# Performance work log

Measured on AMD Instinct MI355X. Metric: run time of the kernel, lower is better.

## Reference

```python
import jax, jax.numpy as jnp
import numpy as np

NUM_HEADS = 8
EMBED_CH = 512   # k channels
OUT_CH = 256     # v channels
MASK_CURRENT = False
NEG_INF = -1e30


def setup_inputs() -> dict:
    key = jax.random.key(0)
    ks = jax.random.split(key, 7)
    N, C, H, W = 8, 256, 32, 32
    s = lambda fan: 1.0 / np.sqrt(fan)
    return {
        "x": jax.random.normal(ks[0], (N, C, H, W), jnp.float32),
        "Wq": jax.random.normal(ks[1], (EMBED_CH, C), jnp.float32) * s(C),
        "bq": jax.random.normal(ks[2], (EMBED_CH,), jnp.float32) * 0.01,
        "Wkv": jax.random.normal(ks[3], (EMBED_CH + OUT_CH, C), jnp.float32) * s(C),
        "bkv": jax.random.normal(ks[4], (EMBED_CH + OUT_CH,), jnp.float32) * 0.01,
        "Wo": jax.random.normal(ks[5], (OUT_CH, OUT_CH), jnp.float32) * s(OUT_CH),
        "bo": jax.random.normal(ks[6], (OUT_CH,), jnp.float32) * 0.01,
    }


def _to_multihead(t, n, T):
    # t: [n, h*d, T] with channel layout '(h d)' -> [n, h, T, d]
    h = NUM_HEADS
    return t.reshape(n, h, -1, T).transpose(0, 1, 3, 2)


def reference(x, Wq, bq, Wkv, bkv, Wo, bo):
    n, C, H, W = x.shape
    T = H * W
    xf = x.reshape(n, C, T)  # flatten spatial dims into sequence

    # 1x1 convs == pointwise channel GEMMs
    q = jnp.einsum('oc,nct->not', Wq, xf) + bq[None, :, None]
    kv = jnp.einsum('oc,nct->not', Wkv, xf) + bkv[None, :, None]
    k, v = kv[:, :EMBED_CH], kv[:, EMBED_CH:]

    q = _to_multihead(q, n, T)   # [n, h, T, dk]
    k = _to_multihead(k, n, T)   # [n, h, T, dk]
    v = _to_multihead(v, n, T)   # [n, h, T, dv]

    dk = k.shape[-1]
    scale = 1.0 / np.sqrt(dk).astype(np.float32)

    # causal mask over flattened spatial positions (lower-triangular)
    diag = -1 if MASK_CURRENT else 0
    mask = jnp.tril(jnp.ones((T, T), dtype=bool), k=diag)  # [T, T]

    attn = jnp.einsum('nhtd,nhsd->nhts', q, k) * scale
    attn = jnp.where(mask[None, None], attn, NEG_INF)
    attn = jax.nn.softmax(attn, axis=-1)
    attn = jnp.where(mask[None, None], attn, 0.0)

    out = jnp.einsum('nhts,nhsd->nhtd', attn, v)            # [n, h, T, dv]
    out = out.transpose(0, 1, 3, 2).reshape(n, OUT_CH, T)   # n (h d) t

    out = jnp.einsum('oc,nct->not', Wo, out) + bo[None, :, None]
    return out.reshape(n, OUT_CH, H, W)
```

## Files before the change

### kernel.cpp

```cpp
#include <hip/hip_runtime.h>
#include <hip/hip_bf16.h>
#include <math.h>

typedef __bf16 bf16;
typedef __attribute__((ext_vector_type(4))) __bf16 bf16x4;
typedef __attribute__((ext_vector_type(8))) __bf16 bf16x8;
typedef __attribute__((ext_vector_type(4))) float f32x4;

#define T_DIM 1024
#define C_DIM 256
#define HEADS 8

static __device__ __forceinline__ int tb(int row, int col) {
  return row * 128 + ((((col >> 3) ^ row) & 7) << 4) + ((col & 7) << 1);
}

__global__ __launch_bounds__(256) void k_prep(const float* __restrict__ x,
    const float* __restrict__ Wq, const float* __restrict__ Wkv, const float* __restrict__ Wo,
    char* __restrict__ xTt, char* __restrict__ Wbt, char* __restrict__ Wot) {
  const int tid = threadIdx.x;
  const int b = blockIdx.x;
  if (b < 512) {
    __shared__ float tile[64][65];
    const int n = b >> 6, rem = b & 63, tt64 = rem >> 2, ct = (rem & 3) << 6;
    const float* xp = x + ((size_t)n * C_DIM + ct) * T_DIM + tt64 * 64;
    const int t4 = (tid & 15) * 4, c0 = tid >> 4;
#pragma unroll
    for (int i = 0; i < 4; ++i) {
      const int c = c0 + i * 16;
      float4 v = *(const float4*)(xp + (size_t)c * T_DIM + t4);
      tile[c][t4] = v.x; tile[c][t4 + 1] = v.y; tile[c][t4 + 2] = v.z; tile[c][t4 + 3] = v.w;
    }
    __syncthreads();
    char* dst = xTt + (((size_t)(n * 8 + (tt64 >> 1))) * 4 + (rem & 3)) * 16384;
    const int rbase = (tt64 & 1) * 64;
#pragma unroll
    for (int i = 0; i < 2; ++i) {
      const int idx = tid + i * 256;
      const int tl = idx >> 3, c8 = (idx & 7) * 8;
      bf16x8 v;
#pragma unroll
      for (int j = 0; j < 8; ++j) v[j] = (bf16)tile[c8 + j][tl];
      *(bf16x8*)(dst + tb(rbase + tl, c8)) = v;
    }
  } else {
    const bool isWo = (b >= 532);
    const int o0 = (b - (isWo ? 532 : 512)) * 64;
#pragma unroll
    for (int i = 0; i < 8; ++i) {
      const int idx = tid + i * 256;
      const int row = idx >> 5, c8 = (idx & 31) * 8;
      const int o = o0 + row;
      const float* src = isWo ? (Wo + (size_t)o * C_DIM + c8)
                              : (o < 512 ? Wq + (size_t)o * C_DIM + c8
                                         : Wkv + (size_t)(o - 512) * C_DIM + c8);
      float4 a = *(const float4*)src;
      float4 bq4 = *(const float4*)(src + 4);
      bf16x8 v;
      v[0]=(bf16)a.x; v[1]=(bf16)a.y; v[2]=(bf16)a.z; v[3]=(bf16)a.w;
      v[4]=(bf16)bq4.x; v[5]=(bf16)bq4.y; v[6]=(bf16)bq4.z; v[7]=(bf16)bq4.w;
      char* base = isWo ? Wot : Wbt;
      char* dst = base + (((size_t)(o >> 7)) * 4 + (c8 >> 6)) * 16384;
      *(bf16x8*)(dst + tb(o & 127, c8 & 63)) = v;
    }
  }
}

__global__ __launch_bounds__(256) void k_qkv(const char* __restrict__ Wbt, const char* __restrict__ xTt,
    const float* __restrict__ bq, const float* __restrict__ bkv,
    bf16* __restrict__ q_ws, char* __restrict__ Kt, char* __restrict__ Vt) {
  __shared__ __attribute__((aligned(128))) unsigned char smem[34816];
  const int tid = threadIdx.x;
  const int nt = blockIdx.x, mt = blockIdx.y, n = blockIdx.z;
  const int w = tid >> 6, lane = tid & 63, lrow = lane & 15, lg = lane >> 4;
  const int wm = (w >> 1) * 64, wn = (w & 1) * 64;
  const char* gA = Wbt + (size_t)mt * 65536;
  const char* gB = xTt + ((size_t)(n * 8 + nt)) * 65536;
  const float s2 = 0.18033688f;
  const int coff = w * 1024 + lane * 16;

  bf16x8 sA0, sA1, sA2, sA3, sB0, sB1, sB2, sB3;
  auto issue = [&](int kk) {
    const char* a = gA + kk * 16384 + coff;
    sA0 = *(const bf16x8*)(a);         sA1 = *(const bf16x8*)(a + 4096);
    sA2 = *(const bf16x8*)(a + 8192);  sA3 = *(const bf16x8*)(a + 12288);
    const char* bsrc = gB + kk * 16384 + coff;
    sB0 = *(const bf16x8*)(bsrc);        sB1 = *(const bf16x8*)(bsrc + 4096);
    sB2 = *(const bf16x8*)(bsrc + 8192); sB3 = *(const bf16x8*)(bsrc + 12288);
  };

  f32x4 acc[4][4] = {};
  issue(0);
#pragma unroll 1
  for (int kk = 0; kk < 4; ++kk) {
    __syncthreads();
    char* da = (char*)smem + coff;
    *(bf16x8*)(da)         = sA0; *(bf16x8*)(da + 4096)  = sA1;
    *(bf16x8*)(da + 8192)  = sA2; *(bf16x8*)(da + 12288) = sA3;
    char* db = (char*)smem + 16384 + coff;
    *(bf16x8*)(db)         = sB0; *(bf16x8*)(db + 4096)  = sB1;
    *(bf16x8*)(db + 8192)  = sB2; *(bf16x8*)(db + 12288) = sB3;
    if (kk < 3) issue(kk + 1);
    __syncthreads();
    const char* As = (const char*)smem;
    const char* Bs = As + 16384;
    bf16x8 af[4][2], bv[4][2];
#pragma unroll
    for (int mi = 0; mi < 4; ++mi)
#pragma unroll
      for (int kh = 0; kh < 2; ++kh)
        af[mi][kh] = *(const bf16x8*)(As + tb(wm + mi * 16 + lrow, kh * 32 + lg * 8));
#pragma unroll
    for (int ni = 0; ni < 4; ++ni)
#pragma unroll
      for (int kh = 0; kh < 2; ++kh)
        bv[ni][kh] = *(const bf16x8*)(Bs + tb(wn + ni * 16 + lrow, kh * 32 + lg * 8));
#pragma unroll
    for (int kh = 0; kh < 2; ++kh)
#pragma unroll
      for (int mi = 0; mi < 4; ++mi)
#pragma unroll
        for (int ni = 0; ni < 4; ++ni)
          acc[mi][ni] = __builtin_amdgcn_mfma_f32_16x16x32_bf16(af[mi][kh], bv[ni][kh], acc[mi][ni], 0, 0, 0);
  }
  __syncthreads();

  const int obase = mt * 128 + wm + lg * 4;
  const int tcol0 = nt * 128 + wn + lrow;
  if (mt < 8) {
#pragma unroll
    for (int mi = 0; mi < 4; ++mi) {
      const int o = obase + mi * 16;
      if (mt < 4) {
        const float4 bb = *(const float4*)(bq + o);
        const int nh = n * 8 + (o >> 6), d = o & 63;
        bf16* qrow = q_ws + (size_t)nh * (T_DIM * 64) + d;
#pragma unroll
        for (int ni = 0; ni < 4; ++ni) {
          const int t = tcol0 + ni * 16;
          f32x4 v = acc[mi][ni];
          bf16x4 pk;
          pk[0]=(bf16)((v[0]+bb.x)*s2); pk[1]=(bf16)((v[1]+bb.y)*s2);
          pk[2]=(bf16)((v[2]+bb.z)*s2); pk[3]=(bf16)((v[3]+bb.w)*s2);
          *(bf16x4*)(qrow + (size_t)t * 64) = pk;
        }
      } else {
        const int o2 = o - 512;
        const float4 bb = *(const float4*)(bkv + o2);
        const int nh = n * 8 + (o2 >> 6), d = o2 & 63;
        char* tbase = Kt + (size_t)nh * 16 * 8192;
#pragma unroll
        for (int ni = 0; ni < 4; ++ni) {
          const int t = tcol0 + ni * 16;
          f32x4 v = acc[mi][ni];
          bf16x4 pk;
          pk[0]=(bf16)(v[0]+bb.x); pk[1]=(bf16)(v[1]+bb.y); pk[2]=(bf16)(v[2]+bb.z); pk[3]=(bf16)(v[3]+bb.w);
          *(bf16x4*)(tbase + (t >> 6) * 8192 + tb(t & 63, d)) = pk;
        }
      }
    }
  } else {
    bf16* tp = (bf16*)smem;
#pragma unroll
    for (int mi = 0; mi < 4; ++mi) {
      const int o3g = (mt - 8) * 128 + wm + mi * 16 + lg * 4;
      const float4 bb = *(const float4*)(bkv + 512 + o3g);
      const float* bbp = (const float*)&bb;
      const int o3l = wm + mi * 16 + lg * 4;
#pragma unroll
      for (int ni = 0; ni < 4; ++ni) {
        const int tl = wn + ni * 16 + lrow;
        f32x4 v = acc[mi][ni];
#pragma unroll
        for (int r = 0; r < 4; ++r)
          tp[(o3l + r) * 132 + tl] = (bf16)(v[r] + bbp[r]);
      }
    }
    __syncthreads();
    const int row = tid >> 1, half = tid & 1;
    const int o3 = (mt - 8) * 128 + row;
    const int nh = n * 8 + (o3 >> 5), dv = o3 & 31;
    char* tile = Vt + (size_t)nh * 16 * 4096 + (nt * 2 + half) * 4096;
    const bf16* src = tp + row * 132 + half * 64;
#pragma unroll
    for (int g = 0; g < 8; ++g) {
      bf16x4 lo = *(const bf16x4*)(src + g * 8);
      bf16x4 hi = *(const bf16x4*)(src + g * 8 + 4);
      bf16x8 vv;
      vv[0]=lo[0]; vv[1]=lo[1]; vv[2]=lo[2]; vv[3]=lo[3];
      vv[4]=hi[0]; vv[5]=hi[1]; vv[6]=hi[2]; vv[7]=hi[3];
      *(bf16x8*)(tile + tb(dv, g * 8)) = vv;
    }
  }
}

__global__ __launch_bounds__(256) void k_attn(const bf16* __restrict__ q_ws,
    const char* __restrict__ Kt, const char* __restrict__ Vt, char* __restrict__ attTt) {
  __shared__ __attribute__((aligned(128))) unsigned char smem[32768];
  const int tid = threadIdx.x;
  const int nh = blockIdx.x, qt = blockIdx.y;
  const int w = tid >> 6, lane = tid & 63, lrow = lane & 15, lg = lane >> 4;
  const int tl = w * 16 + lrow;
  const char* Ktb = Kt + (size_t)nh * 16 * 8192;
  const char* Vtb = Vt + (size_t)nh * 16 * 4096;
  const int n = nh >> 3, h = nh & 7;
  const int coff = tid * 16;

  const int tg = qt * 64 + tl;
  const bf16* qb = q_ws + ((size_t)nh * T_DIM + tg) * 64;
  const bf16x8 qf0 = *(const bf16x8*)(qb + lg * 8);
  const bf16x8 qf1 = *(const bf16x8*)(qb + 32 + lg * 8);

  float l = 0.f;
  f32x4 oa = {}, ob = {};

  bf16x8 s0, s1, s2, s3, s4, s5;
  auto issue = [&](int st2, bool has1) {
    const char* k0 = Ktb + (size_t)st2 * 8192 + coff;
    s0 = *(const bf16x8*)(k0);
    s1 = *(const bf16x8*)(k0 + 4096);
    s4 = *(const bf16x8*)(Vtb + (size_t)st2 * 4096 + coff);
    if (has1) {
      s2 = *(const bf16x8*)(k0 + 8192);
      s3 = *(const bf16x8*)(k0 + 12288);
      s5 = *(const bf16x8*)(Vtb + (size_t)(st2 + 1) * 4096 + coff);
    }
  };

  issue(0, 1 <= qt);
#pragma unroll 1
  for (int st2 = 0; st2 <= qt; st2 += 2) {
    const bool has1 = (st2 + 1 <= qt);
    __syncthreads();
    {
      char* kd = (char*)smem + coff;
      *(bf16x8*)(kd) = s0;
      *(bf16x8*)(kd + 4096) = s1;
      *(bf16x8*)((char*)smem + 16384 + coff) = s4;
      if (has1) {
        *(bf16x8*)(kd + 8192) = s2;
        *(bf16x8*)(kd + 12288) = s3;
        *(bf16x8*)((char*)smem + 20480 + coff) = s5;
      }
    }
    const int nst2 = st2 + 2;
    if (nst2 <= qt) issue(nst2, nst2 + 1 <= qt);
    __syncthreads();
    const int nsub = has1 ? 2 : 1;
#pragma unroll 1
    for (int sub = 0; sub < nsub; ++sub) {
      const int stk = st2 + sub;
      const char* Kbs = (const char*)smem + sub * 8192;
      const char* Vbs = (const char*)smem + 16384 + sub * 4096;
      char* pws = (char*)smem + 24576 + w * 2048;
      const bool diag = (stk == qt);

      f32x4 sacc[4];
      __builtin_amdgcn_s_setprio(1);
#pragma unroll
      for (int rt = 0; rt < 4; ++rt) {
        f32x4 a = {0.f, 0.f, 0.f, 0.f};
        bf16x8 kf0 = *(const bf16x8*)(Kbs + tb(rt * 16 + lrow, lg * 8));
        a = __builtin_amdgcn_mfma_f32_16x16x32_bf16(kf0, qf0, a, 0, 0, 0);
        bf16x8 kf1 = *(const bf16x8*)(Kbs + tb(rt * 16 + lrow, 32 + lg * 8));
        a = __builtin_amdgcn_mfma_f32_16x16x32_bf16(kf1, qf1, a, 0, 0, 0);
        sacc[rt] = a;
      }
      __builtin_amdgcn_s_setprio(0);
      float p[16];
#pragma unroll
      for (int rt = 0; rt < 4; ++rt)
#pragma unroll
        for (int r = 0; r < 4; ++r) {
          float e = __builtin_amdgcn_exp2f(sacc[rt][r]);
          if (diag && (rt * 16 + lg * 4 + r) > tl) e = 0.f;
          p[rt * 4 + r] = e;
        }
      float t0 = (p[0] + p[1]) + (p[2] + p[3]);
      float t1 = (p[4] + p[5]) + (p[6] + p[7]);
      float t2 = (p[8] + p[9]) + (p[10] + p[11]);
      float t3 = (p[12] + p[13]) + (p[14] + p[15]);
      float ps = (t0 + t1) + (t2 + t3);
      ps += __shfl_xor(ps, 16);
      ps += __shfl_xor(ps, 32);
      l += ps;
#pragma unroll
      for (int rt = 0; rt < 4; ++rt) {
        bf16x4 pk;
#pragma unroll
        for (int r = 0; r < 4; ++r) pk[r] = (bf16)p[rt * 4 + r];
        *(bf16x4*)(pws + tb(lrow, rt * 16 + lg * 4)) = pk;
      }
      __builtin_amdgcn_s_setprio(1);
#pragma unroll
      for (int ks = 0; ks < 2; ++ks) {
        bf16x8 pf = *(const bf16x8*)(pws + tb(lrow, ks * 32 + lg * 8));
        bf16x8 vf0 = *(const bf16x8*)(Vbs + tb(lrow, ks * 32 + lg * 8));
        oa = __builtin_amdgcn_mfma_f32_16x16x32_bf16(vf0, pf, oa, 0, 0, 0);
        bf16x8 vf1 = *(const bf16x8*)(Vbs + tb(16 + lrow, ks * 32 + lg * 8));
        ob = __builtin_amdgcn_mfma_f32_16x16x32_bf16(vf1, pf, ob, 0, 0, 0);
      }
      __builtin_amdgcn_s_setprio(0);
    }
  }

  const float inv = 1.0f / l;
  const int ntt = tg >> 7, row = tg & 127;
#pragma unroll
  for (int dt = 0; dt < 2; ++dt) {
    const f32x4 v = dt ? ob : oa;
    const int c = h * 32 + dt * 16 + lg * 4;
    char* tile = attTt + (((size_t)(n * 8 + ntt)) * 4 + (c >> 6)) * 16384;
    bf16x4 pk;
#pragma unroll
    for (int r = 0; r < 4; ++r) pk[r] = (bf16)(v[r] * inv);
    *(bf16x4*)(tile + tb(row, c & 63)) = pk;
  }
}

__global__ __launch_bounds__(256) void k_proj(const char* __restrict__ attTt,
    const char* __restrict__ Wot, const float* __restrict__ bo, float* __restrict__ out) {
  __shared__ __attribute__((aligned(128))) unsigned char smem[12288];
  const int tid = threadIdx.x;
  const int tm = blockIdx.x, om = blockIdx.y, n = blockIdx.z;
  const int w = tid >> 6, lane = tid & 63, lrow = lane & 15, lg = lane >> 4;
  const int wm = (w >> 1) * 16, wn = (w & 1) * 32;
  const char* gA = attTt + ((size_t)(n * 8 + (tm >> 2))) * 65536 + (tm & 3) * 4096;
  const char* gB = Wot + (size_t)(om >> 1) * 65536 + (om & 1) * 8192;
  const int coff = tid * 16;

  bf16x8 pA0, pB0, pB1;
  auto issue = [&](int kk) {
    pA0 = *(const bf16x8*)(gA + kk * 16384 + coff);
    const char* bsrc = gB + kk * 16384 + coff;
    pB0 = *(const bf16x8*)(bsrc); pB1 = *(const bf16x8*)(bsrc + 4096);
  };

  f32x4 acc[2] = {};
  issue(0);
#pragma unroll 1
  for (int kk = 0; kk < 4; ++kk) {
    __syncthreads();
    if (coff < 4096) *(bf16x8*)((char*)smem + coff) = pA0;
    char* db = (char*)smem + 4096 + coff;
    *(bf16x8*)(db) = pB0; *(bf16x8*)(db + 4096) = pB1;
    if (kk < 3) issue(kk + 1);
    __syncthreads();
    const char* As = (const char*)smem;
    const char* Bs = As + 4096;
    bf16x8 af[2], bv[2][2];
#pragma unroll
    for (int kh = 0; kh < 2; ++kh)
      af[kh] = *(const bf16x8*)(As + tb(wm + lrow, kh * 32 + lg * 8));
#pragma unroll
    for (int ni = 0; ni < 2; ++ni)
#pragma unroll
      for (int kh = 0; kh < 2; ++kh)
        bv[ni][kh] = *(const bf16x8*)(Bs + tb(wn + ni * 16 + lrow, kh * 32 + lg * 8));
#pragma unroll
    for (int kh = 0; kh < 2; ++kh)
#pragma unroll
      for (int ni = 0; ni < 2; ++ni)
        acc[ni] = __builtin_amdgcn_mfma_f32_16x16x32_bf16(af[kh], bv[ni][kh], acc[ni], 0, 0, 0);
  }

  const int t0 = tm * 32 + wm + lg * 4;
#pragma unroll
  for (int ni = 0; ni < 2; ++ni) {
    const int o = om * 64 + wn + ni * 16 + lrow;
    const float bb = bo[o];
    f32x4 v = acc[ni];
    v[0] += bb; v[1] += bb; v[2] += bb; v[3] += bb;
    *(f32x4*)(out + ((size_t)(n * C_DIM + o)) * T_DIM + t0) = v;
  }
}

extern "C" void kernel_launch(void* const* d_in, const int* in_sizes, int n_in,
                              void* d_out, int out_size, void* d_ws, size_t ws_size,
                              hipStream_t stream) {
  const float* x   = (const float*)d_in[0];
  const float* Wq  = (const float*)d_in[1];
  const float* bq  = (const float*)d_in[2];
  const float* Wkv = (const float*)d_in[3];
  const float* bkv = (const float*)d_in[4];
  const float* Wo  = (const float*)d_in[5];
  const float* bo  = (const float*)d_in[6];
  float* out = (float*)d_out;

  char* ws = (char*)d_ws;
  char* xTt   = ws;
  char* Wbt   = ws + (4u  << 20);
  char* Wot   = ws + (5u  << 20);
  bf16* q_ws  = (bf16*)(ws + (6u << 20));
  char* Kt    = ws + (14u << 20);
  char* Vt    = ws + (22u << 20);
  char* attTt = ws + (26u << 20);

  k_prep<<<536, 256, 0, stream>>>(x, Wq, Wkv, Wo, xTt, Wbt, Wot);
  k_qkv<<<dim3(8, 10, 8), 256, 0, stream>>>(Wbt, xTt, bq, bkv, q_ws, Kt, Vt);
  k_attn<<<dim3(64, 16), 256, 0, stream>>>(q_ws, Kt, Vt, attTt);
  k_proj<<<dim3(32, 4, 8), 256, 0, stream>>>(attTt, Wot, bo, out);
}
```

Before: 52.44 us.

## Pair causal query tiles per block and read K/V and proj operands directly from global

The attention kernel now gives each block two query tiles (qp and 15-qp), so every block does about the same amount of causal work, and the grid is halved. Each K/V tile is loaded once and used for both query tiles. The LDS staging and its __syncthreads barriers are removed: K/V fragments are read straight from global memory, and LDS holds only the P tiles. The output projection kernel likewise drops LDS staging and reads A/B fragments directly from global. The cost is no explicit prefetch pipeline, more dependence on cache hits, and fewer blocks in flight.

```diff
diff --git a/kernel.cpp b/kernel.cpp
--- a/kernel.cpp
+++ b/kernel.cpp
@@ -196,167 +196,160 @@
 
 __global__ __launch_bounds__(256) void k_attn(const bf16* __restrict__ q_ws,
     const char* __restrict__ Kt, const char* __restrict__ Vt, char* __restrict__ attTt) {
-  __shared__ __attribute__((aligned(128))) unsigned char smem[32768];
+  __shared__ __attribute__((aligned(128))) unsigned char smem[16384];
   const int tid = threadIdx.x;
-  const int nh = blockIdx.x, qt = blockIdx.y;
+  const int nh = blockIdx.x, qp = blockIdx.y;
   const int w = tid >> 6, lane = tid & 63, lrow = lane & 15, lg = lane >> 4;
   const int tl = w * 16 + lrow;
   const char* Ktb = Kt + (size_t)nh * 16 * 8192;
   const char* Vtb = Vt + (size_t)nh * 16 * 4096;
   const int n = nh >> 3, h = nh & 7;
-  const int coff = tid * 16;
-
-  const int tg = qt * 64 + tl;
-  const bf16* qb = q_ws + ((size_t)nh * T_DIM + tg) * 64;
-  const bf16x8 qf0 = *(const bf16x8*)(qb + lg * 8);
-  const bf16x8 qf1 = *(const bf16x8*)(qb + 32 + lg * 8);
-
-  float l = 0.f;
-  f32x4 oa = {}, ob = {};
-
-  bf16x8 s0, s1, s2, s3, s4, s5;
-  auto issue = [&](int st2, bool has1) {
-    const char* k0 = Ktb + (size_t)st2 * 8192 + coff;
-    s0 = *(const bf16x8*)(k0);
-    s1 = *(const bf16x8*)(k0 + 4096);
-    s4 = *(const bf16x8*)(Vtb + (size_t)st2 * 4096 + coff);
-    if (has1) {
-      s2 = *(const bf16x8*)(k0 + 8192);
-      s3 = *(const bf16x8*)(k0 + 12288);
-      s5 = *(const bf16x8*)(Vtb + (size_t)(st2 + 1) * 4096 + coff);
+
+  const int qt0 = qp, qt1 = 15 - qp;
+  const int tg0 = qt0 * 64 + tl, tg1 = qt1 * 64 + tl;
+  const bf16* qb0 = q_ws + ((size_t)nh * T_DIM + tg0) * 64;
+  const bf16* qb1 = q_ws + ((size_t)nh * T_DIM + tg1) * 64;
+  const bf16x8 qA0 = *(const bf16x8*)(qb0 + lg * 8);
+  const bf16x8 qA1 = *(const bf16x8*)(qb0 + 32 + lg * 8);
+  const bf16x8 qB0 = *(const bf16x8*)(qb1 + lg * 8);
+  const bf16x8 qB1 = *(const bf16x8*)(qb1 + 32 + lg * 8);
+
+  char* pwB = (char*)smem + w * 4096;
+  char* pwA = pwB + 2048;
+
+  float l0 = 0.f, l1 = 0.f;
+  f32x4 o0a = {}, o0b = {}, o1a = {}, o1b = {};
+
+  auto smfin = [&](const f32x4* sacc, float& l, char* pws, bool diag) {
+    float p[16];
+#pragma unroll
+    for (int rt = 0; rt < 4; ++rt)
+#pragma unroll
+      for (int r = 0; r < 4; ++r) {
+        float e = __builtin_amdgcn_exp2f(sacc[rt][r]);
+        if (diag && (rt * 16 + lg * 4 + r) > tl) e = 0.f;
+        p[rt * 4 + r] = e;
+      }
+    float t0 = (p[0] + p[1]) + (p[2] + p[3]);
+    float t1 = (p[4] + p[5]) + (p[6] + p[7]);
+    float t2 = (p[8] + p[9]) + (p[10] + p[11]);
+    float t3 = (p[12] + p[13]) + (p[14] + p[15]);
+    float ps = (t0 + t1) + (t2 + t3);
+    ps += __shfl_xor(ps, 16);
+    ps += __shfl_xor(ps, 32);
+    l += ps;
+#pragma unroll
+    for (int rt = 0; rt < 4; ++rt) {
+      bf16x4 pk;
+#pragma unroll
+      for (int r = 0; r < 4; ++r) pk[r] = (bf16)p[rt * 4 + r];
+      *(bf16x4*)(pws + tb(lrow, rt * 16 + lg * 4)) = pk;
     }
   };
 
-  issue(0, 1 <= qt);
 #pragma unroll 1
-  for (int st2 = 0; st2 <= qt; st2 += 2) {
-    const bool has1 = (st2 + 1 <= qt);
-    __syncthreads();
-    {
-      char* kd = (char*)smem + coff;
-      *(bf16x8*)(kd) = s0;
-      *(bf16x8*)(kd + 4096) = s1;
-      *(bf16x8*)((char*)smem + 16384 + coff) = s4;
-      if (has1) {
-        *(bf16x8*)(kd + 8192) = s2;
-        *(bf16x8*)(kd + 12288) = s3;
-        *(bf16x8*)((char*)smem + 20480 + coff) = s5;
-      }
-    }
-    const int nst2 = st2 + 2;
-    if (nst2 <= qt) issue(nst2, nst2 + 1 <= qt);
-    __syncthreads();
-    const int nsub = has1 ? 2 : 1;
-#pragma unroll 1
-    for (int sub = 0; sub < nsub; ++sub) {
-      const int stk = st2 + sub;
-      const char* Kbs = (const char*)smem + sub * 8192;
-      const char* Vbs = (const char*)smem + 16384 + sub * 4096;
-      char* pws = (char*)smem + 24576 + w * 2048;
-      const bool diag = (stk == qt);
-
-      f32x4 sacc[4];
-      __builtin_amdgcn_s_setprio(1);
+  for (int st = 0; st <= qt1; ++st) {
+    const char* Kst = Ktb + (size_t)st * 8192;
+    const char* Vst = Vtb + (size_t)st * 4096;
+    const bool hasA = (st <= qt0);
+
+    bf16x8 kf[4][2];
+#pragma unroll
+    for (int rt = 0; rt < 4; ++rt) {
+      kf[rt][0] = *(const bf16x8*)(Kst + tb(rt * 16 + lrow, lg * 8));
+      kf[rt][1] = *(const bf16x8*)(Kst + tb(rt * 16 + lrow, 32 + lg * 8));
+    }
+
+    f32x4 sB[4], sA[4];
+    __builtin_amdgcn_s_setprio(1);
+#pragma unroll
+    for (int rt = 0; rt < 4; ++rt) {
+      f32x4 a = {0.f, 0.f, 0.f, 0.f};
+      a = __builtin_amdgcn_mfma_f32_16x16x32_bf16(kf[rt][0], qB0, a, 0, 0, 0);
+      a = __builtin_amdgcn_mfma_f32_16x16x32_bf16(kf[rt][1], qB1, a, 0, 0, 0);
+      sB[rt] = a;
+    }
+    if (hasA) {
 #pragma unroll
       for (int rt = 0; rt < 4; ++rt) {
         f32x4 a = {0.f, 0.f, 0.f, 0.f};
-        bf16x8 kf0 = *(const bf16x8*)(Kbs + tb(rt * 16 + lrow, lg * 8));
-        a = __builtin_amdgcn_mfma_f32_16x16x32_bf16(kf0, qf0, a, 0, 0, 0);
-        bf16x8 kf1 = *(const bf16x8*)(Kbs + tb(rt * 16 + lrow, 32 + lg * 8));
-        a = __builtin_amdgcn_mfma_f32_16x16x32_bf16(kf1, qf1, a, 0, 0, 0);
-        sacc[rt] = a;
-      }
-      __builtin_amdgcn_s_setprio(0);
-      float p[16];
-#pragma unroll
-      for (int rt = 0; rt < 4; ++rt)
-#pragma unroll
-        for (int r = 0; r < 4; ++r) {
-          float e = __builtin_amdgcn_exp2f(sacc[rt][r]);
-          if (diag && (rt * 16 + lg * 4 + r) > tl) e = 0.f;
-          p[rt * 4 + r] = e;
-        }
-      float t0 = (p[0] + p[1]) + (p[2] + p[3]);
-      float t1 = (p[4] + p[5]) + (p[6] + p[7]);
-      float t2 = (p[8] + p[9]) + (p[10] + p[11]);
-      float t3 = (p[12] + p[13]) + (p[14] + p[15]);
-      float ps = (t0 + t1) + (t2 + t3);
-      ps += __shfl_xor(ps, 16);
-      ps += __shfl_xor(ps, 32);
-      l += ps;
-#pragma unroll
-      for (int rt = 0; rt < 4; ++rt) {
-        bf16x4 pk;
-#pragma unroll
-        for (int r = 0; r < 4; ++r) pk[r] = (bf16)p[rt * 4 + r];
-        *(bf16x4*)(pws + tb(lrow, rt * 16 + lg * 4)) = pk;
-      }
-      __builtin_amdgcn_s_setprio(1);
+        a = __builtin_amdgcn_mfma_f32_16x16x32_bf16(kf[rt][0], qA0, a, 0, 0, 0);
+        a = __builtin_amdgcn_mfma_f32_16x16x32_bf16(kf[rt][1], qA1, a, 0, 0, 0);
+        sA[rt] = a;
+      }
+    }
+    __builtin_amdgcn_s_setprio(0);
+
+    smfin(sB, l1, pwB, st == qt1);
+    if (hasA) smfin(sA, l0, pwA, st == qt0);
+
+    bf16x8 vf[2][2];
+#pragma unroll
+    for (int ks = 0; ks < 2; ++ks) {
+      vf[ks][0] = *(const bf16x8*)(Vst + tb(lrow, ks * 32 + lg * 8));
+      vf[ks][1] = *(const bf16x8*)(Vst + tb(16 + lrow, ks * 32 + lg * 8));
+    }
+    __builtin_amdgcn_s_setprio(1);
+#pragma unroll
+    for (int ks = 0; ks < 2; ++ks) {
+      bf16x8 pfB = *(const bf16x8*)(pwB + tb(lrow, ks * 32 + lg * 8));
+      o1a = __builtin_amdgcn_mfma_f32_16x16x32_bf16(vf[ks][0], pfB, o1a, 0, 0, 0);
+      o1b = __builtin_amdgcn_mfma_f32_16x16x32_bf16(vf[ks][1], pfB, o1b, 0, 0, 0);
+    }
+    if (hasA) {
 #pragma unroll
       for (int ks = 0; ks < 2; ++ks) {
-        bf16x8 pf = *(const bf16x8*)(pws + tb(lrow, ks * 32 + lg * 8));
-        bf16x8 vf0 = *(const bf16x8*)(Vbs + tb(lrow, ks * 32 + lg * 8));
-        oa = __builtin_amdgcn_mfma_f32_16x16x32_bf16(vf0, pf, oa, 0, 0, 0);
-        bf16x8 vf1 = *(const bf16x8*)(Vbs + tb(16 + lrow, ks * 32 + lg * 8));
-        ob = __builtin_amdgcn_mfma_f32_16x16x32_bf16(vf1, pf, ob, 0, 0, 0);
-      }
-      __builtin_amdgcn_s_setprio(0);
-    }
-  }
-
-  const float inv = 1.0f / l;
-  const int ntt = tg >> 7, row = tg & 127;
-#pragma unroll
-  for (int dt = 0; dt < 2; ++dt) {
-    const f32x4 v = dt ? ob : oa;
-    const int c = h * 32 + dt * 16 + lg * 4;
-    char* tile = attTt + (((size_t)(n * 8 + ntt)) * 4 + (c >> 6)) * 16384;
-    bf16x4 pk;
-#pragma unroll
-    for (int r = 0; r < 4; ++r) pk[r] = (bf16)(v[r] * inv);
-    *(bf16x4*)(tile + tb(row, c & 63)) = pk;
-  }
+        bf16x8 pfA = *(const bf16x8*)(pwA + tb(lrow, ks * 32 + lg * 8));
+        o0a = __builtin_amdgcn_mfma_f32_16x16x32_bf16(vf[ks][0], pfA, o0a, 0, 0, 0);
+        o0b = __builtin_amdgcn_mfma_f32_16x16x32_bf16(vf[ks][1], pfA, o0b, 0, 0, 0);
+      }
+    }
+    __builtin_amdgcn_s_setprio(0);
+  }
+
+  auto epi = [&](int tg, float l, f32x4 oa, f32x4 ob) {
+    const float inv = 1.0f / l;
+    const int ntt = tg >> 7, row = tg & 127;
+#pragma unroll
+    for (int dt = 0; dt < 2; ++dt) {
+      const f32x4 v = dt ? ob : oa;
+      const int c = h * 32 + dt * 16 + lg * 4;
+      char* tile = attTt + (((size_t)(n * 8 + ntt)) * 4 + (c >> 6)) * 16384;
+      bf16x4 pk;
+#pragma unroll
+      for (int r = 0; r < 4; ++r) pk[r] = (bf16)(v[r] * inv);
+      *(bf16x4*)(tile + tb(row, c & 63)) = pk;
+    }
+  };
+  epi(tg0, l0, o0a, o0b);
+  epi(tg1, l1, o1a, o1b);
 }
 
 __global__ __launch_bounds__(256) void k_proj(const char* __restrict__ attTt,
     const char* __restrict__ Wot, const float* __restrict__ bo, float* __restrict__ out) {
-  __shared__ __attribute__((aligned(128))) unsigned char smem[12288];
   const int tid = threadIdx.x;
   const int tm = blockIdx.x, om = blockIdx.y, n = blockIdx.z;
   const int w = tid >> 6, lane = tid & 63, lrow = lane & 15, lg = lane >> 4;
   const int wm = (w >> 1) * 16, wn = (w & 1) * 32;
-  const char* gA = attTt + ((size_t)(n * 8 + (tm >> 2))) * 65536 + (tm & 3) * 4096;
-  const char* gB = Wot + (size_t)(om >> 1) * 65536 + (om & 1) * 8192;
-  const int coff = tid * 16;
-
-  bf16x8 pA0, pB0, pB1;
-  auto issue = [&](int kk) {
-    pA0 = *(const bf16x8*)(gA + kk * 16384 + coff);
-    const char* bsrc = gB + kk * 16384 + coff;
-    pB0 = *(const bf16x8*)(bsrc); pB1 = *(const bf16x8*)(bsrc + 4096);
-  };
+  const char* gA = attTt + ((size_t)(n * 8 + (tm >> 2))) * 65536;
+  const int arow = (tm & 3) * 32 + wm + lrow;
+  const char* gB = Wot + (size_t)(om >> 1) * 65536;
+  const int brow = (om & 1) * 64 + wn + lrow;
 
   f32x4 acc[2] = {};
-  issue(0);
-#pragma unroll 1
+#pragma unroll
   for (int kk = 0; kk < 4; ++kk) {
-    __syncthreads();
-    if (coff < 4096) *(bf16x8*)((char*)smem + coff) = pA0;
-    char* db = (char*)smem + 4096 + coff;
-    *(bf16x8*)(db) = pB0; *(bf16x8*)(db + 4096) = pB1;
-    if (kk < 3) issue(kk + 1);
-    __syncthreads();
-    const char* As = (const char*)smem;
-    const char* Bs = As + 4096;
+    const char* At = gA + kk * 16384;
+    const char* Bt = gB + kk * 16384;
     bf16x8 af[2], bv[2][2];
 #pragma unroll
     for (int kh = 0; kh < 2; ++kh)
-      af[kh] = *(const bf16x8*)(As + tb(wm + lrow, kh * 32 + lg * 8));
+      af[kh] = *(const bf16x8*)(At + tb(arow, kh * 32 + lg * 8));
 #pragma unroll
     for (int ni = 0; ni < 2; ++ni)
 #pragma unroll
       for (int kh = 0; kh < 2; ++kh)
-        bv[ni][kh] = *(const bf16x8*)(Bs + tb(wn + ni * 16 + lrow, kh * 32 + lg * 8));
+        bv[ni][kh] = *(const bf16x8*)(Bt + tb(brow + ni * 16, kh * 32 + lg * 8));
 #pragma unroll
     for (int kh = 0; kh < 2; ++kh)
 #pragma unroll
@@ -398,6 +391,6 @@
 
   k_prep<<<536, 256, 0, stream>>>(x, Wq, Wkv, Wo, xTt, Wbt, Wot);
   k_qkv<<<dim3(8, 10, 8), 256, 0, stream>>>(Wbt, xTt, bq, bkv, q_ws, Kt, Vt);
-  k_attn<<<dim3(64, 16), 256, 0, stream>>>(q_ws, Kt, Vt, attTt);
+  k_attn<<<dim3(64, 8), 256, 0, stream>>>(q_ws, Kt, Vt, attTt);
   k_proj<<<dim3(32, 4, 8), 256, 0, stream>>>(attTt, Wot, bo, out);
 }
```

After: 55.12 us. 5.1% more time.
